# Kernel optimization log

Hardware: AMD Instinct MI355X
Metric: run time of the kernel (lower is better)

The kernel has to match this reference:

```python
import jax, jax.numpy as jnp
import numpy as np

B, CIN, COUT, H, W = 16, 64, 64, 256, 256
M1, M2 = 32, 32


def setup_inputs() -> dict:
    key = jax.random.key(0)
    k = jax.random.split(key, 7)
    x = jax.random.normal(k[0], (B, CIN, H, W), dtype=jnp.float32)
    # emulate int8 quantized weights: stored values in [-128, 127]
    q_weights1 = jax.random.randint(k[1], (CIN, COUT, M1, M2, 2), -128, 128, dtype=jnp.int32)
    q_weights2 = jax.random.randint(k[2], (CIN, COUT, M1, M2, 2), -128, 128, dtype=jnp.int32)
    w1_scale = jax.random.uniform(k[3], (1,), dtype=jnp.float32) * 0.01 + 0.001
    w1_min = jax.random.normal(k[4], (1,), dtype=jnp.float32) * 0.1
    w2_scale = jax.random.uniform(k[5], (1,), dtype=jnp.float32) * 0.01 + 0.001
    w2_min = jax.random.normal(k[6], (1,), dtype=jnp.float32) * 0.1
    return {"x": x, "q_weights1": q_weights1, "q_weights2": q_weights2,
            "w1_scale": w1_scale, "w1_min": w1_min,
            "w2_scale": w2_scale, "w2_min": w2_min}


def _dequant_complex(q, scale, min_val):
    # (q + 127) * scale + min, then view last dim (re, im) as complex
    w = (q.astype(jnp.float32) + 127.0) * scale + min_val
    return jax.lax.complex(w[..., 0], w[..., 1])


def reference(x, q_weights1, q_weights2, w1_scale, w1_min, w2_scale, w2_min):
    b, cin, h, w = x.shape
    # rfft2 with ortho norm, complex64
    x_ft = jnp.fft.rfft2(x, norm="ortho")  # [B, Cin, H, W//2+1]

    w1c = _dequant_complex(q_weights1, w1_scale[0], w1_min[0])  # [Cin, Cout, M1, M2]
    w2c = _dequant_complex(q_weights2, w2_scale[0], w2_min[0])

    # complex multiply + channel contraction on the retained low/high modes
    out1 = jnp.einsum("bixy,ioxy->boxy", x_ft[:, :, :M1, :M2], w1c)
    out2 = jnp.einsum("bixy,ioxy->boxy", x_ft[:, :, h - M1:, :M2], w2c)

    out_ft = jnp.zeros((b, COUT, h, w // 2 + 1), dtype=x_ft.dtype)
    out_ft = out_ft.at[:, :, :M1, :M2].set(out1)
    out_ft = out_ft.at[:, :, h - M1:, :M2].set(out2)

    return jnp.fft.irfft2(out_ft, s=(h, w), norm="ortho")  # [B, Cout, H, W] float32
```

## Files before the change

### kernel.cpp

```cpp
#include <hip/hip_runtime.h>
#include <math.h>

#define NB 16
#define NCIN 64
#define NCOUT 64
#define NH 256
#define NW 256
#define NM 64
#define NKX 32
#define INV256 (1.0f/256.0f)

typedef __attribute__((ext_vector_type(8))) short short8v;
typedef __attribute__((ext_vector_type(4))) float f32x4;
typedef unsigned short u16;
typedef unsigned int u32;

__device__ __forceinline__ void bf16_split(float v, u16& hi, u16& lo) {
    u32 b = __float_as_uint(v);
    u32 hib = b & 0xffff0000u;
    float lof = v - __uint_as_float(hib);
    hi = (u16)(hib >> 16);
    lo = (u16)(__float_as_uint(lof) >> 16);
}

__device__ __forceinline__ u16 bf16_rtn(float v) {
    u32 b = __float_as_uint(v);
    u32 r = b + 0x7fffu + ((b >> 16) & 1u);
    return (u16)(r >> 16);
}

__global__ __launch_bounds__(256) void init_tw(u16* __restrict__ tw) {
    const int tid = blockIdx.x * 256 + threadIdx.x;
    const float TWO_PI = 6.28318530717958647692f;
    if (tid < 16384) {
        const int e = tid & 7, lane = (tid >> 3) & 63;
        const int nt = (tid >> 9) & 3, kc = tid >> 11;
        const int w = kc * 32 + (lane >> 4) * 8 + e;
        const int n = nt * 16 + (lane & 15);
        const int kx = n >> 1, p = n & 1;
        const float ang = TWO_PI * (float)((kx * w) & 255) * INV256;
        const float v = p ? -sinf(ang) : cosf(ang);
        u16 hi, lo; bf16_split(v, hi, lo);
        tw[tid] = hi; tw[16384 + tid] = lo;
    } else {
        const int u = tid - 16384;
        const int e = u & 7, lane = (u >> 3) & 63;
        const int kc = (u >> 9) & 7, mt = u >> 12;
        const int m = mt * 16 + (lane & 15);
        const int h = kc * 32 + (lane >> 4) * 8 + e;
        const int ky = (m < 32) ? m : (192 + m);
        const float ang = TWO_PI * (float)((ky * h) & 255) * INV256;
        const float c = cosf(ang), s = sinf(ang);
        u16 hi, lo;
        bf16_split(c,  hi, lo); tw[32768 + u] = hi; tw[49152 + u]  = lo;
        bf16_split(s,  hi, lo); tw[65536 + u] = hi; tw[81920 + u]  = lo;
        bf16_split(-s, hi, lo); tw[98304 + u] = hi; tw[114688 + u] = lo;
    }
}

__global__ __launch_bounds__(256) void init_tw2(u16* __restrict__ tw2) {
    const int tid = blockIdx.x * 256 + threadIdx.x;
    const float TWO_PI = 6.28318530717958647692f;
    if (tid < 16384) {
        const int e = tid & 7, lane = (tid >> 3) & 63;
        const int kc = (tid >> 9) & 1, HT = tid >> 10;
        const int h = HT * 16 + (lane & 15);
        const int m = kc * 32 + ((lane >> 4) << 3) + e;
        const int ky = (m < 32) ? m : (192 + m);
        const float ang = TWO_PI * (float)((ky * h) & 255) * INV256;
        tw2[tid]         = bf16_rtn(cosf(ang));
        tw2[16384 + tid] = bf16_rtn(sinf(ang));
        tw2[32768 + tid] = bf16_rtn(-sinf(ang));
    } else {
        const int u = tid - 16384;
        const int e = u & 7, lane = (u >> 3) & 63;
        const int kc = (u >> 9) & 1, nt = u >> 10;
        const int w = nt * 16 + (lane & 15);
        const int kk = kc * 32 + ((lane >> 4) << 3) + e;
        const int kx = kk >> 1, c = kk & 1;
        const float wt = (kx == 0) ? 1.f : 2.f;
        const float ang = TWO_PI * (float)((kx * w) & 255) * INV256;
        const float v = c ? (-wt * sinf(ang) * INV256) : (wt * cosf(ang) * INV256);
        tw2[49152 + u] = bf16_rtn(v);
    }
}

__global__ __launch_bounds__(256) void fwd_mfma(const float* __restrict__ x,
                                                const u16* __restrict__ tw,
                                                float2* __restrict__ xft) {
    __shared__ u16 planes[4 * 32 * 264];
    const int t = threadIdx.x;
    const int lane = t & 63;
    const int wv = t >> 6;
    const int l15 = lane & 15;
    const int lk = lane >> 4;
    const float* __restrict__ xb = x + (size_t)blockIdx.x * (NH * NW);

    const u16* __restrict__ T1h = tw;
    const u16* __restrict__ T1l = tw + 16384;

    for (int mt = 0; mt < 4; ++mt) {
        const int hbase = wv * 64 + mt * 16;
        f32x4 acc[4] = {f32x4{0,0,0,0}, f32x4{0,0,0,0}, f32x4{0,0,0,0}, f32x4{0,0,0,0}};
        for (int kc = 0; kc < 8; ++kc) {
            const float* xr = xb + (size_t)(hbase + l15) * NW + kc * 32 + lk * 8;
            const float4 xa = *(const float4*)xr;
            const float4 xc = *(const float4*)(xr + 4);
            const float v[8] = {xa.x, xa.y, xa.z, xa.w, xc.x, xc.y, xc.z, xc.w};
            short8v Ah, Al;
            #pragma unroll
            for (int e = 0; e < 8; ++e) {
                u16 hi, lo; bf16_split(v[e], hi, lo);
                Ah[e] = (short)hi; Al[e] = (short)lo;
            }
            const int tbase = (kc * 4) * 512 + lane * 8;
            #pragma unroll
            for (int nt = 0; nt < 4; ++nt) {
                const short8v Bh = *(const short8v*)(T1h + tbase + nt * 512);
                const short8v Bl = *(const short8v*)(T1l + tbase + nt * 512);
                acc[nt] = __builtin_amdgcn_mfma_f32_16x16x32_bf16(Ah, Bh, acc[nt], 0, 0, 0);
                acc[nt] = __builtin_amdgcn_mfma_f32_16x16x32_bf16(Ah, Bl, acc[nt], 0, 0, 0);
                acc[nt] = __builtin_amdgcn_mfma_f32_16x16x32_bf16(Al, Bh, acc[nt], 0, 0, 0);
            }
        }
        #pragma unroll
        for (int nt = 0; nt < 4; ++nt) {
            const int n = nt * 16 + l15;
            const int kx = n >> 1, p = n & 1;
            #pragma unroll
            for (int r = 0; r < 4; ++r) {
                const int h = hbase + lk * 4 + r;
                u16 hi, lo; bf16_split(acc[nt][r], hi, lo);
                planes[(2 * p) * 8448 + kx * 264 + h] = hi;
                planes[(2 * p + 1) * 8448 + kx * 264 + h] = lo;
            }
        }
    }
    __syncthreads();

    const u16* __restrict__ C2h = tw + 32768;
    const u16* __restrict__ C2l = tw + 49152;
    const u16* __restrict__ S2h = tw + 65536;
    const u16* __restrict__ S2l = tw + 81920;
    const u16* __restrict__ Snh = tw + 98304;
    const u16* __restrict__ Snl = tw + 114688;

    f32x4 zre[2] = {f32x4{0,0,0,0}, f32x4{0,0,0,0}};
    f32x4 zim[2] = {f32x4{0,0,0,0}, f32x4{0,0,0,0}};
    for (int kc = 0; kc < 8; ++kc) {
        const int abase = (wv * 8 + kc) * 512 + lane * 8;
        const short8v Ch = *(const short8v*)(C2h + abase);
        const short8v Cl = *(const short8v*)(C2l + abase);
        const short8v Sh = *(const short8v*)(S2h + abase);
        const short8v Sl = *(const short8v*)(S2l + abase);
        const short8v Nh = *(const short8v*)(Snh + abase);
        const short8v Nl = *(const short8v*)(Snl + abase);
        #pragma unroll
        for (int nt = 0; nt < 2; ++nt) {
            const int kx = nt * 16 + l15;
            const int off = kx * 264 + kc * 32 + lk * 8;
            const short8v Yrh = *(const short8v*)(planes + off);
            const short8v Yrl = *(const short8v*)(planes + 8448 + off);
            const short8v Yih = *(const short8v*)(planes + 16896 + off);
            const short8v Yil = *(const short8v*)(planes + 25344 + off);
            zre[nt] = __builtin_amdgcn_mfma_f32_16x16x32_bf16(Ch, Yrh, zre[nt], 0, 0, 0);
            zre[nt] = __builtin_amdgcn_mfma_f32_16x16x32_bf16(Ch, Yrl, zre[nt], 0, 0, 0);
            zre[nt] = __builtin_amdgcn_mfma_f32_16x16x32_bf16(Cl, Yrh, zre[nt], 0, 0, 0);
            zre[nt] = __builtin_amdgcn_mfma_f32_16x16x32_bf16(Sh, Yih, zre[nt], 0, 0, 0);
            zre[nt] = __builtin_amdgcn_mfma_f32_16x16x32_bf16(Sh, Yil, zre[nt], 0, 0, 0);
            zre[nt] = __builtin_amdgcn_mfma_f32_16x16x32_bf16(Sl, Yih, zre[nt], 0, 0, 0);
            zim[nt] = __builtin_amdgcn_mfma_f32_16x16x32_bf16(Ch, Yih, zim[nt], 0, 0, 0);
            zim[nt] = __builtin_amdgcn_mfma_f32_16x16x32_bf16(Ch, Yil, zim[nt], 0, 0, 0);
            zim[nt] = __builtin_amdgcn_mfma_f32_16x16x32_bf16(Cl, Yih, zim[nt], 0, 0, 0);
            zim[nt] = __builtin_amdgcn_mfma_f32_16x16x32_bf16(Nh, Yrh, zim[nt], 0, 0, 0);
            zim[nt] = __builtin_amdgcn_mfma_f32_16x16x32_bf16(Nh, Yrl, zim[nt], 0, 0, 0);
            zim[nt] = __builtin_amdgcn_mfma_f32_16x16x32_bf16(Nl, Yrh, zim[nt], 0, 0, 0);
        }
    }
    float2* __restrict__ op = xft + (size_t)blockIdx.x * (NM * NKX);
    #pragma unroll
    for (int nt = 0; nt < 2; ++nt) {
        const int kx = nt * 16 + l15;
        #pragma unroll
        for (int r = 0; r < 4; ++r) {
            const int m = wv * 16 + lk * 4 + r;
            op[m * NKX + kx] = make_float2(zre[nt][r] * INV256, zim[nt][r] * INV256);
        }
    }
}

__global__ __launch_bounds__(256) void mode_v6(const float2* __restrict__ xft,
                                               const int* __restrict__ q1,
                                               const int* __restrict__ q2,
                                               const float* __restrict__ w1s,
                                               const float* __restrict__ w1m,
                                               const float* __restrict__ w2s,
                                               const float* __restrict__ w2m,
                                               float2* __restrict__ oft) {
    __shared__ float2 xs[16 * 65 * 4];
    __shared__ float2 wsd[4 * 64 * 16];
    const int m  = blockIdx.x;
    const int og = blockIdx.y;
    const int kh = blockIdx.z;
    const int t = threadIdx.x;
    const int mm = (m < 32) ? m : (m - 32);
    const int* __restrict__ q = (m < 32) ? q1 : q2;
    const float scale = (m < 32) ? w1s[0] : w2s[0];
    const float wmin  = (m < 32) ? w1m[0] : w2m[0];

    const float4* __restrict__ xf4 = (const float4*)xft;
    #pragma unroll
    for (int rep = 0; rep < 4; ++rep) {
        const int p = rep * 256 + t;
        const int b = p >> 6, i = p & 63;
        const float4 a0 = xf4[(size_t)p * 1024 + m * 16 + kh * 2];
        const float4 a1 = xf4[(size_t)p * 1024 + m * 16 + kh * 2 + 1];
        float4* dst = (float4*)&xs[(b * 65 + i) * 4];
        dst[0] = a0; dst[1] = a1;
    }
    const int4* __restrict__ qi4 = (const int4*)q;
    #pragma unroll
    for (int rep = 0; rep < 4; ++rep) {
        const int p = rep * 256 + t;
        const int i = p >> 4, o = p & 15;
        const size_t base = ((size_t)(i * 64 + og * 16 + o) * 1024 + mm * 32 + kh * 4) >> 1;
        const int4 w0 = qi4[base];
        const int4 w1 = qi4[base + 1];
        wsd[(0 * 64 + i) * 16 + o] = make_float2(((float)w0.x + 127.f) * scale + wmin,
                                                 ((float)w0.y + 127.f) * scale + wmin);
        wsd[(1 * 64 + i) * 16 + o] = make_float2(((float)w0.z + 127.f) * scale + wmin,
                                                 ((float)w0.w + 127.f) * scale + wmin);
        wsd[(2 * 64 + i) * 16 + o] = make_float2(((float)w1.x + 127.f) * scale + wmin,
                                                 ((float)w1.y + 127.f) * scale + wmin);
        wsd[(3 * 64 + i) * 16 + o] = make_float2(((float)w1.z + 127.f) * scale + wmin,
                                                 ((float)w1.w + 127.f) * scale + wmin);
    }
    __syncthreads();

    const int b = t >> 4, o = t & 15;
    float accr[4], acci[4];
    #pragma unroll
    for (int k = 0; k < 4; ++k) { accr[k] = 0.f; acci[k] = 0.f; }

    #pragma unroll 4
    for (int i = 0; i < 64; ++i) {
        const float2* xr = &xs[(b * 65 + i) * 4];
        #pragma unroll
        for (int k = 0; k < 4; ++k) {
            const float2 xv = xr[k];
            const float2 wv = wsd[(k * 64 + i) * 16 + o];
            accr[k] += xv.x * wv.x - xv.y * wv.y;
            acci[k] += xv.x * wv.y + xv.y * wv.x;
        }
    }

    float2* __restrict__ op = oft + ((size_t)(b * 64 + og * 16 + o) * NM + m) * NKX + kh * 4;
    #pragma unroll
    for (int k = 0; k < 4; ++k) op[k] = make_float2(accr[k], acci[k]);
}

__global__ __launch_bounds__(256) void inv_mfma(const float2* __restrict__ oft,
                                                const u16* __restrict__ tw2,
                                                float* __restrict__ out) {
    __shared__ u16 lds[9216];
    const int t = threadIdx.x;
    const int lane = t & 63;
    const int wv = t >> 6;
    const int l15 = lane & 15;
    const int lk = lane >> 4;
    const int hh = blockIdx.y;

    const float2* __restrict__ ip = oft + (size_t)blockIdx.x * (NM * NKX);
    #pragma unroll
    for (int r = 0; r < 8; ++r) {
        const int idx = r * 256 + t;
        const int m = idx >> 5, kx = idx & 31;
        const float2 v = ip[idx];
        lds[kx * 72 + m]        = bf16_rtn(v.x);
        lds[2304 + kx * 72 + m] = bf16_rtn(v.y);
    }
    __syncthreads();

    const u16* __restrict__ C4 = tw2;
    const u16* __restrict__ S4 = tw2 + 16384;
    const u16* __restrict__ N4 = tw2 + 32768;

    short8v Br[2][2], Bi[2][2];
    #pragma unroll
    for (int nt = 0; nt < 2; ++nt) {
        #pragma unroll
        for (int kc = 0; kc < 2; ++kc) {
            const int off = (nt * 16 + l15) * 72 + kc * 32 + lk * 8;
            Br[nt][kc] = *(const short8v*)(lds + off);
            Bi[nt][kc] = *(const short8v*)(lds + 2304 + off);
        }
    }

    {
        const int lt = wv;
        const int HT = hh * 4 + wv;
        f32x4 zr[2] = {f32x4{0,0,0,0}, f32x4{0,0,0,0}};
        f32x4 zi[2] = {f32x4{0,0,0,0}, f32x4{0,0,0,0}};
        #pragma unroll
        for (int kc = 0; kc < 2; ++kc) {
            const int abase = ((HT * 2 + kc) * 64 + lane) * 8;
            const short8v C = *(const short8v*)(C4 + abase);
            const short8v S = *(const short8v*)(S4 + abase);
            const short8v N = *(const short8v*)(N4 + abase);
            #pragma unroll
            for (int nt = 0; nt < 2; ++nt) {
                zr[nt] = __builtin_amdgcn_mfma_f32_16x16x32_bf16(C, Br[nt][kc], zr[nt], 0, 0, 0);
                zr[nt] = __builtin_amdgcn_mfma_f32_16x16x32_bf16(N, Bi[nt][kc], zr[nt], 0, 0, 0);
                zi[nt] = __builtin_amdgcn_mfma_f32_16x16x32_bf16(S, Br[nt][kc], zi[nt], 0, 0, 0);
                zi[nt] = __builtin_amdgcn_mfma_f32_16x16x32_bf16(C, Bi[nt][kc], zi[nt], 0, 0, 0);
            }
        }
        #pragma unroll
        for (int nt = 0; nt < 2; ++nt) {
            const int kx = nt * 16 + l15;
            #pragma unroll
            for (int r = 0; r < 4; ++r) {
                const int hl = lt * 16 + lk * 4 + r;
                const u32 pk = (u32)bf16_rtn(zr[nt][r]) | ((u32)bf16_rtn(zi[nt][r]) << 16);
                *(u32*)(lds + 4608 + hl * 72 + 2 * kx) = pk;
            }
        }
    }
    __syncthreads();

    const u16* __restrict__ W5 = tw2 + 49152;
    float* __restrict__ op = out + (size_t)blockIdx.x * (NH * NW) + (size_t)hh * 64 * NW;
    for (int nt = 0; nt < 16; ++nt) {
        const short8v B0 = *(const short8v*)(W5 + ((nt * 2 + 0) * 64 + lane) * 8);
        const short8v B1 = *(const short8v*)(W5 + ((nt * 2 + 1) * 64 + lane) * 8);
        const int w = nt * 16 + l15;
        {
            const int lt = wv;
            const int h0 = lt * 16 + l15;
            const short8v A0 = *(const short8v*)(lds + 4608 + h0 * 72 + lk * 8);
            const short8v A1 = *(const short8v*)(lds + 4608 + h0 * 72 + 32 + lk * 8);
            f32x4 acc = {0, 0, 0, 0};
            acc = __builtin_amdgcn_mfma_f32_16x16x32_bf16(A0, B0, acc, 0, 0, 0);
            acc = __builtin_amdgcn_mfma_f32_16x16x32_bf16(A1, B1, acc, 0, 0, 0);
            #pragma unroll
            for (int r = 0; r < 4; ++r) {
                const int hl = lt * 16 + lk * 4 + r;
                op[hl * 256 + w] = acc[r];
            }
        }
    }
}

extern "C" void kernel_launch(void* const* d_in, const int* in_sizes, int n_in,
                              void* d_out, int out_size, void* d_ws, size_t ws_size,
                              hipStream_t stream) {
    const float* x  = (const float*)d_in[0];
    const int* q1   = (const int*)d_in[1];
    const int* q2   = (const int*)d_in[2];
    const float* w1s = (const float*)d_in[3];
    const float* w1m = (const float*)d_in[4];
    const float* w2s = (const float*)d_in[5];
    const float* w2m = (const float*)d_in[6];
    float* out = (float*)d_out;

    float2* xft = (float2*)d_ws;
    float2* oft = xft + (size_t)NB * NCIN * NM * NKX;
    u16* tw  = (u16*)((char*)d_ws + (size_t)48 * 1024 * 1024);
    u16* tw2 = tw + 131072;

    init_tw<<<128, 256, 0, stream>>>(tw);
    init_tw2<<<128, 256, 0, stream>>>(tw2);
    fwd_mfma<<<NB * NCIN, 256, 0, stream>>>(x, tw, xft);
    mode_v6<<<dim3(NM, 4, 8), 256, 0, stream>>>(xft, q1, q2, w1s, w1m, w2s, w2m, oft);
    inv_mfma<<<dim3(NB * NCOUT, 4), 256, 0, stream>>>(oft, tw2, out);
}
```

Before: 239.8 us.

## Double-buffer mode-mixing loads and widen per-block tiles in inverse kernel

The mode-mixing kernel now streams input channels in eight chunks through double-buffered shared memory with register prefetch, and gives each thread eight kx modes instead of four. The grid is halved along kh and the kernel uses padded float4 layouts. The inverse kernel handles 128 output rows per block instead of 64, so each wave runs two M-tiles and the block count is halved. The aim is to hide global load latency and amortize the shared setup of the B fragments, at the cost of more LDS and registers and fewer blocks.

```diff
diff --git a/kernel.cpp b/kernel.cpp
--- a/kernel.cpp
+++ b/kernel.cpp
@@ -189,7 +189,7 @@
     }
 }
 
-__global__ __launch_bounds__(256) void mode_v6(const float2* __restrict__ xft,
+__global__ __launch_bounds__(256) void mode_v8(const float2* __restrict__ xft,
                                                const int* __restrict__ q1,
                                                const int* __restrict__ q2,
                                                const float* __restrict__ w1s,
@@ -197,72 +197,92 @@
                                                const float* __restrict__ w2s,
                                                const float* __restrict__ w2m,
                                                float2* __restrict__ oft) {
-    __shared__ float2 xs[16 * 65 * 4];
-    __shared__ float2 wsd[4 * 64 * 16];
+    __shared__ float2 xs[2][8][16][8];
+    __shared__ float2 ws[2][8][16][10];
     const int m  = blockIdx.x;
     const int og = blockIdx.y;
     const int kh = blockIdx.z;
     const int t = threadIdx.x;
+    const int b = t >> 4, o = t & 15;
     const int mm = (m < 32) ? m : (m - 32);
     const int* __restrict__ q = (m < 32) ? q1 : q2;
     const float scale = (m < 32) ? w1s[0] : w2s[0];
     const float wmin  = (m < 32) ? w1m[0] : w2m[0];
 
+    const int row = t >> 1;
+    const int il = row >> 4, rb = row & 15, half = t & 1;
+
     const float4* __restrict__ xf4 = (const float4*)xft;
-    #pragma unroll
-    for (int rep = 0; rep < 4; ++rep) {
-        const int p = rep * 256 + t;
-        const int b = p >> 6, i = p & 63;
-        const float4 a0 = xf4[(size_t)p * 1024 + m * 16 + kh * 2];
-        const float4 a1 = xf4[(size_t)p * 1024 + m * 16 + kh * 2 + 1];
-        float4* dst = (float4*)&xs[(b * 65 + i) * 4];
-        dst[0] = a0; dst[1] = a1;
-    }
-    const int4* __restrict__ qi4 = (const int4*)q;
-    #pragma unroll
-    for (int rep = 0; rep < 4; ++rep) {
-        const int p = rep * 256 + t;
-        const int i = p >> 4, o = p & 15;
-        const size_t base = ((size_t)(i * 64 + og * 16 + o) * 1024 + mm * 32 + kh * 4) >> 1;
-        const int4 w0 = qi4[base];
-        const int4 w1 = qi4[base + 1];
-        wsd[(0 * 64 + i) * 16 + o] = make_float2(((float)w0.x + 127.f) * scale + wmin,
-                                                 ((float)w0.y + 127.f) * scale + wmin);
-        wsd[(1 * 64 + i) * 16 + o] = make_float2(((float)w0.z + 127.f) * scale + wmin,
-                                                 ((float)w0.w + 127.f) * scale + wmin);
-        wsd[(2 * 64 + i) * 16 + o] = make_float2(((float)w1.x + 127.f) * scale + wmin,
-                                                 ((float)w1.y + 127.f) * scale + wmin);
-        wsd[(3 * 64 + i) * 16 + o] = make_float2(((float)w1.z + 127.f) * scale + wmin,
-                                                 ((float)w1.w + 127.f) * scale + wmin);
-    }
+    const int4*   __restrict__ qi4 = (const int4*)q;
+    const size_t xbase = (size_t)(rb * 64 + il) * 1024 + m * 16 + kh * 4 + half * 2;
+    const size_t wbase = (size_t)(il * 64 + og * 16 + rb) * 512 + mm * 16 + kh * 4 + half * 2;
+
+    float4 px0, px1; int4 pw0, pw1;
+
+    #define MV8_LOAD(P)                                                        \
+        px0 = xf4[xbase + (size_t)(P) * 8 * 1024];                             \
+        px1 = xf4[xbase + (size_t)(P) * 8 * 1024 + 1];                         \
+        pw0 = qi4[wbase + (size_t)(P) * 8 * 32768];                            \
+        pw1 = qi4[wbase + (size_t)(P) * 8 * 32768 + 1];
+
+    #define MV8_WRITE(BUF)                                                     \
+        {                                                                      \
+            float4* xd = (float4*)&xs[BUF][il][rb][half * 4];                  \
+            xd[0] = px0; xd[1] = px1;                                          \
+            float4* wd = (float4*)&ws[BUF][il][rb][half * 4];                  \
+            wd[0] = make_float4(((float)pw0.x + 127.f) * scale + wmin,         \
+                                ((float)pw0.y + 127.f) * scale + wmin,         \
+                                ((float)pw0.z + 127.f) * scale + wmin,         \
+                                ((float)pw0.w + 127.f) * scale + wmin);        \
+            wd[1] = make_float4(((float)pw1.x + 127.f) * scale + wmin,         \
+                                ((float)pw1.y + 127.f) * scale + wmin,         \
+                                ((float)pw1.z + 127.f) * scale + wmin,         \
+                                ((float)pw1.w + 127.f) * scale + wmin);        \
+        }
+
+    MV8_LOAD(0)
+    MV8_WRITE(0)
     __syncthreads();
 
-    const int b = t >> 4, o = t & 15;
-    float accr[4], acci[4];
-    #pragma unroll
-    for (int k = 0; k < 4; ++k) { accr[k] = 0.f; acci[k] = 0.f; }
-
-    #pragma unroll 4
-    for (int i = 0; i < 64; ++i) {
-        const float2* xr = &xs[(b * 65 + i) * 4];
-        #pragma unroll
-        for (int k = 0; k < 4; ++k) {
-            const float2 xv = xr[k];
-            const float2 wv = wsd[(k * 64 + i) * 16 + o];
-            accr[k] += xv.x * wv.x - xv.y * wv.y;
-            acci[k] += xv.x * wv.y + xv.y * wv.x;
-        }
-    }
-
-    float2* __restrict__ op = oft + ((size_t)(b * 64 + og * 16 + o) * NM + m) * NKX + kh * 4;
-    #pragma unroll
-    for (int k = 0; k < 4; ++k) op[k] = make_float2(accr[k], acci[k]);
+    float accr[8], acci[8];
+    #pragma unroll
+    for (int k = 0; k < 8; ++k) { accr[k] = 0.f; acci[k] = 0.f; }
+
+    #pragma unroll 1
+    for (int p = 0; p < 8; ++p) {
+        const int cur = p & 1;
+        if (p < 7) { MV8_LOAD(p + 1) }
+        #pragma unroll
+        for (int jl = 0; jl < 8; ++jl) {
+            const float4* xr4 = (const float4*)&xs[cur][jl][b][0];
+            const float4* wr4 = (const float4*)&ws[cur][jl][o][0];
+            #pragma unroll
+            for (int kq = 0; kq < 4; ++kq) {
+                const float4 xv = xr4[kq];
+                const float4 wv = wr4[kq];
+                accr[2 * kq]     += xv.x * wv.x - xv.y * wv.y;
+                acci[2 * kq]     += xv.x * wv.y + xv.y * wv.x;
+                accr[2 * kq + 1] += xv.z * wv.z - xv.w * wv.w;
+                acci[2 * kq + 1] += xv.z * wv.w + xv.w * wv.z;
+            }
+        }
+        if (p < 7) {
+            MV8_WRITE(cur ^ 1)
+            __syncthreads();
+        }
+    }
+    #undef MV8_LOAD
+    #undef MV8_WRITE
+
+    float2* __restrict__ op = oft + ((size_t)(b * 64 + og * 16 + o) * NM + m) * NKX + kh * 8;
+    #pragma unroll
+    for (int k = 0; k < 8; ++k) op[k] = make_float2(accr[k], acci[k]);
 }
 
 __global__ __launch_bounds__(256) void inv_mfma(const float2* __restrict__ oft,
                                                 const u16* __restrict__ tw2,
                                                 float* __restrict__ out) {
-    __shared__ u16 lds[9216];
+    __shared__ u16 lds[13824];
     const int t = threadIdx.x;
     const int lane = t & 63;
     const int wv = t >> 6;
@@ -296,9 +316,10 @@
         }
     }
 
-    {
-        const int lt = wv;
-        const int HT = hh * 4 + wv;
+    #pragma unroll
+    for (int mt = 0; mt < 2; ++mt) {
+        const int lt = wv * 2 + mt;
+        const int HT = hh * 8 + lt;
         f32x4 zr[2] = {f32x4{0,0,0,0}, f32x4{0,0,0,0}};
         f32x4 zi[2] = {f32x4{0,0,0,0}, f32x4{0,0,0,0}};
         #pragma unroll
@@ -329,13 +350,14 @@
     __syncthreads();
 
     const u16* __restrict__ W5 = tw2 + 49152;
-    float* __restrict__ op = out + (size_t)blockIdx.x * (NH * NW) + (size_t)hh * 64 * NW;
+    float* __restrict__ op = out + (size_t)blockIdx.x * (NH * NW) + (size_t)hh * 128 * NW;
     for (int nt = 0; nt < 16; ++nt) {
         const short8v B0 = *(const short8v*)(W5 + ((nt * 2 + 0) * 64 + lane) * 8);
         const short8v B1 = *(const short8v*)(W5 + ((nt * 2 + 1) * 64 + lane) * 8);
         const int w = nt * 16 + l15;
-        {
-            const int lt = wv;
+        #pragma unroll
+        for (int mt = 0; mt < 2; ++mt) {
+            const int lt = wv * 2 + mt;
             const int h0 = lt * 16 + l15;
             const short8v A0 = *(const short8v*)(lds + 4608 + h0 * 72 + lk * 8);
             const short8v A1 = *(const short8v*)(lds + 4608 + h0 * 72 + 32 + lk * 8);
@@ -371,6 +393,6 @@
     init_tw<<<128, 256, 0, stream>>>(tw);
     init_tw2<<<128, 256, 0, stream>>>(tw2);
     fwd_mfma<<<NB * NCIN, 256, 0, stream>>>(x, tw, xft);
-    mode_v6<<<dim3(NM, 4, 8), 256, 0, stream>>>(xft, q1, q2, w1s, w1m, w2s, w2m, oft);
-    inv_mfma<<<dim3(NB * NCOUT, 4), 256, 0, stream>>>(oft, tw2, out);
-}
+    mode_v8<<<dim3(NM, 4, 4), 256, 0, stream>>>(xft, q1, q2, w1s, w1m, w2s, w2m, oft);
+    inv_mfma<<<dim3(NB * NCOUT, 2), 256, 0, stream>>>(oft, tw2, out);
+}
```

Result: no change. 240.8 us (+0.4%).
